# Optimization experiments

Measured on AMD Instinct MI355X. Metric: run time of the kernel, lower is better.

The kernel has to match this reference:

```python
import jax, jax.numpy as jnp
import numpy as np

COMMITMENT_COST = 0.25

def setup_inputs() -> dict:
    key = jax.random.key(0)
    k1, k2 = jax.random.split(key)
    z = jax.random.normal(k1, (8, 2048, 768), dtype=jnp.float32)
    # codebook initialized uniform(-1/K, 1/K) in the original; use same scale
    K = 2048
    emb = jax.random.uniform(k2, (K, 768), dtype=jnp.float32, minval=-1.0 / K, maxval=1.0 / K)
    return {"z": z, "emb": emb}

def reference(z, emb):
    B, S, D = z.shape
    z_flat = z.reshape(-1, D)                                   # [N, D]
    # squared-euclidean distances via expansion: ||z||^2 + ||e||^2 - 2 z e^T
    distances = (
        jnp.sum(z_flat * z_flat, axis=1, keepdims=True)
        + jnp.sum(emb * emb, axis=1)
        - 2.0 * jnp.matmul(z_flat, emb.T)
    )                                                           # [N, K]
    ids_flat = jnp.argmin(distances, axis=1)                    # [N]
    z_q = emb[ids_flat].reshape(z.shape)                        # gather + reshape
    concept_ids = ids_flat.reshape(B, S)
    # training path with use_ema=True: codebook_loss = 0, commitment term only.
    # NOTE: original (faithfully) computes mse(z.detach(), z_q) — grad flows to z_q.
    commitment_loss = jnp.mean((jax.lax.stop_gradient(z) - z_q) ** 2)
    vq_loss = COMMITMENT_COST * commitment_loss
    # straight-through estimator
    z_q_st = z + jax.lax.stop_gradient(z_q - z)
    return z_q_st, concept_ids, vq_loss
```

## Files before the change

kernel.cpp:

```cpp
#include <hip/hip_runtime.h>
#include <float.h>

typedef unsigned short ushort_t;
typedef unsigned int uint_t;

#define NROWS 16384
#define DDIM  768
#define KCODES 2048
#define NCB    16
#define MARGIN 8e-4f

__device__ __forceinline__ ushort_t f2bf(float x) {
    uint_t u = __float_as_uint(x);
    uint_t r = (u + 0x7fffu + ((u >> 16) & 1u)) >> 16;
    return (ushort_t)r;
}
__device__ __forceinline__ float bf2f(ushort_t h) {
    return __uint_as_float(((uint_t)h) << 16);
}

__global__ void prep_emb(const float* __restrict__ emb, float* __restrict__ ee,
                         ushort_t* __restrict__ Eh) {
    int c = blockIdx.x;
    const float* e = emb + (size_t)c * DDIM;
    int t = threadIdx.x;
    float s = 0.f;
    for (int i = t; i < DDIM; i += 256) { float v = e[i]; s += v * v; }
    for (int off = 32; off; off >>= 1) s += __shfl_down(s, off);
    __shared__ float red[4];
    if ((t & 63) == 0) red[t >> 6] = s;
    __syncthreads();
    if (t == 0) ee[c] = red[0] + red[1] + red[2] + red[3];
    if (t < 192) {
        const float4 v = ((const float4*)e)[t];
        ushort4 h;
        h.x = f2bf(v.x); h.y = f2bf(v.y); h.z = f2bf(v.z); h.w = f2bf(v.w);
        ((ushort4*)(Eh + (size_t)c * DDIM))[t] = h;
    }
}

__global__ void prep_z(const float* __restrict__ z, float* __restrict__ zz,
                       ushort_t* __restrict__ Zh) {
    const int t = threadIdx.x;
    const int row = blockIdx.x * 4 + (t >> 6);
    const int lane = t & 63;
    const float* zr = z + (size_t)row * DDIM;
    float s = 0.f;
    for (int i = lane; i < DDIM; i += 64) { float v = zr[i]; s += v * v; }
    for (int off = 32; off; off >>= 1) s += __shfl_down(s, off);
    if (lane == 0) zz[row] = s;
    const float4* zr4 = (const float4*)zr;
    ushort4* dh = (ushort4*)(Zh + (size_t)row * DDIM);
    #pragma unroll
    for (int j = 0; j < 3; ++j) {
        const int i4 = lane + 64 * j;
        const float4 v = zr4[i4];
        ushort4 h;
        h.x = f2bf(v.x); h.y = f2bf(v.y); h.z = f2bf(v.z); h.w = f2bf(v.w);
        dh[i4] = h;
    }
}

typedef __attribute__((ext_vector_type(8))) short bf16x8;
typedef __attribute__((ext_vector_type(4))) float f32x4;

__device__ __forceinline__ int swz(int r) { return (r & 3) ^ ((r >> 2) & 3); }

__global__ __launch_bounds__(256)
void mfma_kernel(const ushort_t* __restrict__ Ab, const ushort_t* __restrict__ Bb,
                 const float* __restrict__ ee, float* __restrict__ bmin,
                 float2* __restrict__ slots) {
    __shared__ __align__(16) char smem[32768];
    ushort_t* Als = (ushort_t*)smem;
    ushort_t* Bls = (ushort_t*)(smem + 16384);
    float* rowmin = (float*)smem;
    int*   rcnt   = (int*)(smem + 512);
    float (*sval)[8] = (float(*)[8])(smem + 1024);
    int   (*sidx)[8] = (int(*)[8])(smem + 5120);

    const int t = threadIdx.x;
    const int w = t >> 6, l = t & 63;
    const int bx = blockIdx.x & 127, by = blockIdx.x >> 7;
    const int row0 = bx << 7, col0 = by << 7;

    f32x4 acc[4][4];
    #pragma unroll
    for (int i = 0; i < 4; ++i)
        #pragma unroll
        for (int j = 0; j < 4; ++j) acc[i][j] = (f32x4){0.f, 0.f, 0.f, 0.f};

    const int sri  = l >> 2;
    const int slot = l & 3;
    const int rha = (w & 1) << 6;
    const int rhb = (w >> 1) << 6;

    for (int kt = 0; kt < 12; ++kt) {
        const int kb = kt << 6;
        __syncthreads();
        #pragma unroll
        for (int s = 0; s < 2; ++s) {
            #pragma unroll
            for (int q = 0; q < 2; ++q) {
                const int r0 = ((w << 1) + q) << 4;
                const int ra = r0 + sri;
                const int c  = slot ^ swz(ra);
                const int kk = kb + (s << 5) + (c << 3);
                const ushort_t* gpa = Ab + (size_t)(row0 + ra) * DDIM + kk;
                __builtin_amdgcn_global_load_lds(
                    (const __attribute__((address_space(1))) void*)gpa,
                    (__attribute__((address_space(3))) void*)(smem + (s << 13) + (r0 << 6)),
                    16, 0, 0);
                const ushort_t* gpb = Bb + (size_t)(col0 + ra) * DDIM + kk;
                __builtin_amdgcn_global_load_lds(
                    (const __attribute__((address_space(1))) void*)gpb,
                    (__attribute__((address_space(3))) void*)(smem + 16384 + (s << 13) + (r0 << 6)),
                    16, 0, 0);
            }
        }
        __syncthreads();

        #pragma unroll
        for (int s = 0; s < 2; ++s) {
            bf16x8 af[4], bfr[4];
            #pragma unroll
            for (int mi = 0; mi < 4; ++mi) {
                const int r = rha + (mi << 4) + (l & 15);
                const int sw = (l >> 4) ^ swz(r);
                af[mi] = *(const bf16x8*)&Als[(s << 12) + (r << 5) + (sw << 3)];
            }
            #pragma unroll
            for (int ni = 0; ni < 4; ++ni) {
                const int r = rhb + (ni << 4) + (l & 15);
                const int sw = (l >> 4) ^ swz(r);
                bfr[ni] = *(const bf16x8*)&Bls[(s << 12) + (r << 5) + (sw << 3)];
            }
            #pragma unroll
            for (int mi = 0; mi < 4; ++mi)
                #pragma unroll
                for (int ni = 0; ni < 4; ++ni)
                    acc[mi][ni] = __builtin_amdgcn_mfma_f32_16x16x32_bf16(
                        af[mi], bfr[ni], acc[mi][ni], 0, 0, 0);
        }
    }
    __syncthreads();

    float ecv[4];
    #pragma unroll
    for (int ni = 0; ni < 4; ++ni) ecv[ni] = ee[col0 + rhb + (ni << 4) + (l & 15)];
    #pragma unroll
    for (int mi = 0; mi < 4; ++mi)
        #pragma unroll
        for (int ni = 0; ni < 4; ++ni)
            #pragma unroll
            for (int r = 0; r < 4; ++r)
                acc[mi][ni][r] = ecv[ni] - 2.0f * acc[mi][ni][r];

    float vmr[4][4];
    #pragma unroll
    for (int mi = 0; mi < 4; ++mi)
        #pragma unroll
        for (int r = 0; r < 4; ++r) {
            float v = fminf(fminf(acc[mi][0][r], acc[mi][1][r]),
                            fminf(acc[mi][2][r], acc[mi][3][r]));
            v = fminf(v, __shfl_xor(v, 1));
            v = fminf(v, __shfl_xor(v, 2));
            v = fminf(v, __shfl_xor(v, 4));
            v = fminf(v, __shfl_xor(v, 8));
            vmr[mi][r] = v;
        }

    if (t < 128) { rowmin[t] = FLT_MAX; rcnt[t] = 0; }
    __syncthreads();
    if (w < 2 && (l & 15) == 0) {
        #pragma unroll
        for (int mi = 0; mi < 4; ++mi)
            #pragma unroll
            for (int r = 0; r < 4; ++r)
                rowmin[rha + (mi << 4) + ((l >> 4) << 2) + r] = vmr[mi][r];
    }
    __syncthreads();
    if (w >= 2 && (l & 15) == 0) {
        #pragma unroll
        for (int mi = 0; mi < 4; ++mi)
            #pragma unroll
            for (int r = 0; r < 4; ++r) {
                const int m = rha + (mi << 4) + ((l >> 4) << 2) + r;
                rowmin[m] = fminf(rowmin[m], vmr[mi][r]);
            }
    }
    __syncthreads();

    #pragma unroll
    for (int mi = 0; mi < 4; ++mi)
        #pragma unroll
        for (int r = 0; r < 4; ++r) {
            const int m = rha + (mi << 4) + ((l >> 4) << 2) + r;
            const float lim = rowmin[m] + MARGIN;
            #pragma unroll
            for (int ni = 0; ni < 4; ++ni) {
                const float vv = acc[mi][ni][r];
                if (vv <= lim) {
                    const int p = atomicAdd(&rcnt[m], 1);
                    if (p < 8) {
                        sval[m][p] = vv;
                        sidx[m][p] = col0 + rhb + (ni << 4) + (l & 15);
                    }
                }
            }
        }
    __syncthreads();

    if (t < 128) {
        const int row = row0 + t;
        bmin[(size_t)by * NROWS + row] = rowmin[t];
        const int n = rcnt[t] < 8 ? rcnt[t] : 8;
        float2 rec[8];
        #pragma unroll
        for (int s2 = 0; s2 < 8; ++s2)
            rec[s2] = (s2 < n) ? make_float2(sval[t][s2], __int_as_float(sidx[t][s2]))
                               : make_float2(FLT_MAX, __int_as_float(0x7fffffff));
        float4* dst = (float4*)(slots + ((size_t)by * NROWS + row) * 8);
        dst[0] = make_float4(rec[0].x, rec[0].y, rec[1].x, rec[1].y);
        dst[1] = make_float4(rec[2].x, rec[2].y, rec[3].x, rec[3].y);
        dst[2] = make_float4(rec[4].x, rec[4].y, rec[5].x, rec[5].y);
        dst[3] = make_float4(rec[6].x, rec[6].y, rec[7].x, rec[7].y);
    }
}

__global__ __launch_bounds__(256)
void combine_select_gather(const float* __restrict__ bmin, const float2* __restrict__ slots,
                           const float* __restrict__ ee, const float* __restrict__ zz,
                           const float* __restrict__ z, const float* __restrict__ emb,
                           float* __restrict__ ids_f32, float* __restrict__ out0,
                           float* __restrict__ rowloss) {
    const int t = threadIdx.x;
    const int row = blockIdx.x * 4 + (t >> 6);
    const int l = t & 63;

    float v = (l < NCB) ? bmin[(size_t)l * NROWS + row] : FLT_MAX;
    v = fminf(v, __shfl_xor(v, 8));
    v = fminf(v, __shfl_xor(v, 4));
    v = fminf(v, __shfl_xor(v, 2));
    v = fminf(v, __shfl_xor(v, 1));
    const float T = __shfl(v, 0) + MARGIN;

    const int blk = l >> 2;
    const int s0 = (l << 1) & 7;
    const float2* sp = slots + ((size_t)blk * NROWS + row) * 8 + s0;
    const float2 a  = sp[0];
    const float2 b2 = sp[1];

    unsigned long long m0 = __ballot(a.x <= T);
    unsigned long long m1 = __ballot(b2.x <= T);

    const float zzr = zz[row];
    const float* zr = z + (size_t)row * DDIM;

    float bestd = FLT_MAX; int besti = 0x7fffffff;
    while (m0 | m1) {
        int j; float iv;
        if (m0) { j = __ffsll(m0) - 1; m0 &= m0 - 1; iv = a.y; }
        else    { j = __ffsll(m1) - 1; m1 &= m1 - 1; iv = b2.y; }
        const int idx = __float_as_int(__shfl(iv, j));
        const float* er = emb + (size_t)idx * DDIM;
        float p = 0.f;
        #pragma unroll
        for (int k = 0; k < 12; ++k) p += zr[l + 64 * k] * er[l + 64 * k];
        for (int off = 32; off; off >>= 1) p += __shfl_down(p, off);
        if (l == 0) {
            const float t1 = zzr + ee[idx];
            const float d  = t1 - 2.0f * p;
            if (d < bestd || (d == bestd && idx < besti)) { bestd = d; besti = idx; }
        }
    }
    const int bi = __shfl(besti, 0);
    if (l == 0) ids_f32[row] = (float)bi;

    const float4* zr4 = (const float4*)zr;
    const float4* er4 = (const float4*)(emb + (size_t)bi * DDIM);
    float4* o4 = (float4*)(out0 + (size_t)row * DDIM);
    float s = 0.f;
    #pragma unroll
    for (int j = 0; j < 3; ++j) {
        const int i4 = l + 64 * j;
        const float4 zv = zr4[i4];
        const float4 ev = er4[i4];
        float4 o;
        o.x = zv.x + (ev.x - zv.x); o.y = zv.y + (ev.y - zv.y);
        o.z = zv.z + (ev.z - zv.z); o.w = zv.w + (ev.w - zv.w);
        o4[i4] = o;
        const float dx = zv.x - ev.x, dy = zv.y - ev.y;
        const float dz = zv.z - ev.z, dw = zv.w - ev.w;
        s += dx * dx + dy * dy + dz * dz + dw * dw;
    }
    for (int off = 32; off; off >>= 1) s += __shfl_down(s, off);
    if (l == 0) rowloss[row] = s;
}

__global__ void loss16k_kernel(const float* __restrict__ rowloss, float* __restrict__ out_loss) {
    const int t = threadIdx.x;
    double s = 0.0;
    for (int i = t; i < NROWS; i += 256) s += (double)rowloss[i];
    for (int off = 32; off; off >>= 1) s += __shfl_down(s, off);
    __shared__ double red[4];
    if ((t & 63) == 0) red[t >> 6] = s;
    __syncthreads();
    if (t == 0) {
        const double total = red[0] + red[1] + red[2] + red[3];
        out_loss[0] = (float)(0.25 * (total / (double)((size_t)NROWS * DDIM)));
    }
}

__global__ void ee_kernel(const float* __restrict__ emb, float* __restrict__ ee) {
    int c = blockIdx.x;
    const float* e = emb + (size_t)c * DDIM;
    int t = threadIdx.x;
    float s = 0.f;
    for (int i = t; i < DDIM; i += 256) { float v = e[i]; s += v * v; }
    for (int off = 32; off; off >>= 1) s += __shfl_down(s, off);
    __shared__ float red[4];
    if ((t & 63) == 0) red[t >> 6] = s;
    __syncthreads();
    if (t == 0) ee[c] = red[0] + red[1] + red[2] + red[3];
}

__global__ void zz_kernel(const float* __restrict__ z, float* __restrict__ zz) {
    const int t = threadIdx.x;
    const int row = blockIdx.x * 4 + (t >> 6);
    const int lane = t & 63;
    const float* zr = z + (size_t)row * DDIM;
    float s = 0.f;
    for (int i = lane; i < DDIM; i += 64) { float v = zr[i]; s += v * v; }
    for (int off = 32; off; off >>= 1) s += __shfl_down(s, off);
    if (lane == 0) zz[row] = s;
}

#define BM 32
#define BN 128
#define BKS 32
#define SPLITC 2
#define CODES_PER_BLOCK (KCODES / SPLITC)
#define NCHUNK (CODES_PER_BLOCK / BN)
#define NSTAGE (DDIM / BKS)
#define APADR 33
#define BPADC 132

__global__ __launch_bounds__(256)
void argmin_kernel(const float* __restrict__ z, const float* __restrict__ emb,
                   const float* __restrict__ ee, const float* __restrict__ zz,
                   float* __restrict__ pval, int* __restrict__ pidx) {
    __shared__ float Af[BKS][APADR];
    __shared__ float Bf[BKS][BPADC];
    __shared__ float cval[BM][33];
    __shared__ int   cidx[BM][33];
    __shared__ float zzs[BM];
    const int t = threadIdx.x;
    const int part = blockIdx.x & (SPLITC - 1);
    const int rb = blockIdx.x >> 1;
    const int row0 = rb * BM;
    const int cbase = part * CODES_PER_BLOCK;
    const int tx = t & 31, ty = t >> 5;
    const int sr = t >> 3;
    const int sk = 4 * (t & 7);
    if (t < BM) zzs[t] = zz[row0 + t];
    float bv[4]; int bi[4];
    #pragma unroll
    for (int i = 0; i < 4; ++i) { bv[i] = FLT_MAX; bi[i] = 0x7fffffff; }
    const float* zt = z + (size_t)(row0 + sr) * DDIM;
    for (int chunk = 0; chunk < NCHUNK; ++chunk) {
        const int c0 = cbase + chunk * BN;
        const float* ebase = emb + (size_t)(c0 + sr) * DDIM;
        float acc[4][4];
        #pragma unroll
        for (int i = 0; i < 4; ++i)
            #pragma unroll
            for (int j = 0; j < 4; ++j) acc[i][j] = 0.f;
        float4 pa = *(const float4*)&zt[sk];
        float4 pb[4];
        #pragma unroll
        for (int m = 0; m < 4; ++m) pb[m] = *(const float4*)&ebase[(size_t)(32 * m) * DDIM + sk];
        for (int s = 0; s < NSTAGE; ++s) {
            __syncthreads();
            Af[sk + 0][sr] = pa.x; Af[sk + 1][sr] = pa.y;
            Af[sk + 2][sr] = pa.z; Af[sk + 3][sr] = pa.w;
            #pragma unroll
            for (int m = 0; m < 4; ++m) {
                Bf[sk + 0][sr + 32 * m] = pb[m].x;
                Bf[sk + 1][sr + 32 * m] = pb[m].y;
                Bf[sk + 2][sr + 32 * m] = pb[m].z;
                Bf[sk + 3][sr + 32 * m] = pb[m].w;
            }
            __syncthreads();
            if (s + 1 < NSTAGE) {
                const int k1 = (s + 1) * BKS + sk;
                pa = *(const float4*)&zt[k1];
                #pragma unroll
                for (int m = 0; m < 4; ++m)
                    pb[m] = *(const float4*)&ebase[(size_t)(32 * m) * DDIM + k1];
            }
            #pragma unroll
            for (int kk = 0; kk < BKS; ++kk) {
                const float4 a4 = *(const float4*)&Af[kk][4 * ty];
                const float4 b4 = *(const float4*)&Bf[kk][4 * tx];
                const float aa[4] = {a4.x, a4.y, a4.z, a4.w};
                const float bb[4] = {b4.x, b4.y, b4.z, b4.w};
                #pragma unroll
                for (int i = 0; i < 4; ++i)
                    #pragma unroll
                    for (int j = 0; j < 4; ++j) acc[i][j] += aa[i] * bb[j];
            }
        }
        const float4 e4 = *(const float4*)&ee[c0 + 4 * tx];
        const float eev[4] = {e4.x, e4.y, e4.z, e4.w};
        #pragma unroll
        for (int i = 0; i < 4; ++i) {
            const float zzr = zzs[4 * ty + i];
            #pragma unroll
            for (int j = 0; j < 4; ++j) {
                const int code = c0 + 4 * tx + j;
                const float t1 = zzr + eev[j];
                const float d  = t1 - 2.0f * acc[i][j];
                if (d < bv[i] || (d == bv[i] && code < bi[i])) { bv[i] = d; bi[i] = code; }
            }
        }
    }
    __syncthreads();
    #pragma unroll
    for (int i = 0; i < 4; ++i) { cval[4 * ty + i][tx] = bv[i]; cidx[4 * ty + i][tx] = bi[i]; }
    __syncthreads();
    if (t < BM) {
        float v = FLT_MAX; int id = 0x7fffffff;
        #pragma unroll
        for (int x = 0; x < 32; ++x) {
            const float cv = cval[t][x]; const int ci = cidx[t][x];
            if (cv < v || (cv == v && ci < id)) { v = cv; id = ci; }
        }
        pval[part * NROWS + row0 + t] = v;
        pidx[part * NROWS + row0 + t] = id;
    }
}

__global__ void combine_kernel(const float* __restrict__ pval, const int* __restrict__ pidx,
                               float* __restrict__ ids_f32) {
    const int r = blockIdx.x * 256 + threadIdx.x;
    float v = pval[r];           int id = pidx[r];
    const float v1 = pval[NROWS + r]; const int i1 = pidx[NROWS + r];
    if (v1 < v || (v1 == v && i1 < id)) { v = v1; id = i1; }
    ids_f32[r] = (float)id;
}

__global__ __launch_bounds__(256)
void gather_kernel(const float* __restrict__ z, const float* __restrict__ emb,
                   const float* __restrict__ ids_f32, float* __restrict__ out0,
                   float* __restrict__ part) {
    const int b = blockIdx.x;
    const int t = threadIdx.x;
    const int rl = t >> 4, c = t & 15;
    __shared__ int ids[16];
    if (t < 16) ids[t] = (int)ids_f32[b * 16 + t];
    __syncthreads();
    const int row = b * 16 + rl;
    const float4* zr = (const float4*)(z + (size_t)row * DDIM);
    float4* orow = (float4*)(out0 + (size_t)row * DDIM);
    const float4* er = (const float4*)(emb + (size_t)ids[rl] * DDIM);
    float s = 0.f;
    #pragma unroll
    for (int j = 0; j < 12; ++j) {
        const int i4 = c + 16 * j;
        const float4 zv = zr[i4];
        const float4 ev = er[i4];
        float4 o;
        o.x = zv.x + (ev.x - zv.x); o.y = zv.y + (ev.y - zv.y);
        o.z = zv.z + (ev.z - zv.z); o.w = zv.w + (ev.w - zv.w);
        orow[i4] = o;
        float dx = zv.x - ev.x, dy = zv.y - ev.y, dz = zv.z - ev.z, dw = zv.w - ev.w;
        s += dx * dx + dy * dy + dz * dz + dw * dw;
    }
    for (int off = 32; off; off >>= 1) s += __shfl_down(s, off);
    __shared__ float red[4];
    if ((t & 63) == 0) red[t >> 6] = s;
    __syncthreads();
    if (t == 0) part[b] = red[0] + red[1] + red[2] + red[3];
}

__global__ void loss_kernel(const float* __restrict__ part, float* __restrict__ out_loss) {
    const int t = threadIdx.x;
    double s = 0.0;
    for (int i = t; i < 1024; i += 256) s += (double)part[i];
    for (int off = 32; off; off >>= 1) s += __shfl_down(s, off);
    __shared__ double red[4];
    if ((t & 63) == 0) red[t >> 6] = s;
    __syncthreads();
    if (t == 0) {
        const double total = red[0] + red[1] + red[2] + red[3];
        out_loss[0] = (float)(0.25 * (total / (double)((size_t)NROWS * DDIM)));
    }
}

#define EE_OFF   0
#define ZZ_OFF   8192
#define RL_OFF   73728
#define EH_OFF   139264
#define ZH_OFF   (EH_OFF + (size_t)KCODES * DDIM * 2)
#define BMIN_OFF (ZH_OFF + (size_t)NROWS * DDIM * 2)
#define SLOT_OFF (BMIN_OFF + (size_t)NCB * NROWS * 4)
#define WS_NEED  (SLOT_OFF + (size_t)NCB * NROWS * 8 * 8)
#define PV_OFF   81920

extern "C" void kernel_launch(void* const* d_in, const int* in_sizes, int n_in,
                              void* d_out, int out_size, void* d_ws, size_t ws_size,
                              hipStream_t stream) {
    const float* z   = (const float*)d_in[0];
    const float* emb = (const float*)d_in[1];

    float* out0     = (float*)d_out;
    float* out_ids  = out0 + (size_t)NROWS * DDIM;
    float* out_loss = out_ids + NROWS;

    char* ws = (char*)d_ws;
    float* ee   = (float*)(ws + EE_OFF);
    float* zzws = (float*)(ws + ZZ_OFF);

    if (ws_size >= WS_NEED) {
        ushort_t* Eh   = (ushort_t*)(ws + EH_OFF);
        ushort_t* Zh   = (ushort_t*)(ws + ZH_OFF);
        float*    bmin = (float*)(ws + BMIN_OFF);
        float2*   slot = (float2*)(ws + SLOT_OFF);
        float*    rl   = (float*)(ws + RL_OFF);
        prep_emb<<<KCODES, 256, 0, stream>>>(emb, ee, Eh);
        prep_z<<<NROWS / 4, 256, 0, stream>>>(z, zzws, Zh);
        mfma_kernel<<<(NROWS / 128) * NCB, 256, 0, stream>>>(Zh, Eh, ee, bmin, slot);
        combine_select_gather<<<NROWS / 4, 256, 0, stream>>>(bmin, slot, ee, zzws, z, emb,
                                                             out_ids, out0, rl);
        loss16k_kernel<<<1, 256, 0, stream>>>(rl, out_loss);
    } else {
        float* part = (float*)(ws + RL_OFF);
        float* pval = (float*)(ws + PV_OFF);
        int*   pidx = (int*)(ws + PV_OFF + 131072);
        ee_kernel<<<KCODES, 256, 0, stream>>>(emb, ee);
        zz_kernel<<<NROWS / 4, 256, 0, stream>>>(z, zzws);
        argmin_kernel<<<(NROWS / BM) * SPLITC, 256, 0, stream>>>(z, emb, ee, zzws, pval, pidx);
        combine_kernel<<<NROWS / 256, 256, 0, stream>>>(pval, pidx, out_ids);
        gather_kernel<<<NROWS / 16, 256, 0, stream>>>(z, emb, out_ids, out0, part);
        loss_kernel<<<1, 256, 0, stream>>>(part, out_loss);
    }
}
```

Measured before the change: 249.3 us.

## Widen MFMA tiles to 128x256, merge prep kernels, fold loss via atomics

The MFMA argmin kernel now covers 256 codebook columns per block instead of 128, which halves the column splits and the partial-min/slot traffic. Its K loop switches to single-stage 32-wide steps with precomputed load and LDS addresses, and sets launch bounds for two blocks per CU. The two prep kernels are merged into one launch, and the final loss reduction kernel is dropped in favour of per-block float atomicAdd. In exchange there is more register pressure from 32 accumulators, less K work per barrier, and a loss sum in nondeterministic float order.

```diff
diff --git a/kernel.cpp b/kernel.cpp
--- a/kernel.cpp
+++ b/kernel.cpp
@@ -7,7 +7,7 @@
 #define NROWS 16384
 #define DDIM  768
 #define KCODES 2048
-#define NCB    16
+#define NCB2   8
 #define MARGIN 8e-4f
 
 __device__ __forceinline__ ushort_t f2bf(float x) {
@@ -19,45 +19,47 @@
     return __uint_as_float(((uint_t)h) << 16);
 }
 
-__global__ void prep_emb(const float* __restrict__ emb, float* __restrict__ ee,
-                         ushort_t* __restrict__ Eh) {
-    int c = blockIdx.x;
-    const float* e = emb + (size_t)c * DDIM;
-    int t = threadIdx.x;
-    float s = 0.f;
-    for (int i = t; i < DDIM; i += 256) { float v = e[i]; s += v * v; }
-    for (int off = 32; off; off >>= 1) s += __shfl_down(s, off);
-    __shared__ float red[4];
-    if ((t & 63) == 0) red[t >> 6] = s;
-    __syncthreads();
-    if (t == 0) ee[c] = red[0] + red[1] + red[2] + red[3];
-    if (t < 192) {
-        const float4 v = ((const float4*)e)[t];
-        ushort4 h;
-        h.x = f2bf(v.x); h.y = f2bf(v.y); h.z = f2bf(v.z); h.w = f2bf(v.w);
-        ((ushort4*)(Eh + (size_t)c * DDIM))[t] = h;
-    }
-}
-
-__global__ void prep_z(const float* __restrict__ z, float* __restrict__ zz,
-                       ushort_t* __restrict__ Zh) {
-    const int t = threadIdx.x;
-    const int row = blockIdx.x * 4 + (t >> 6);
-    const int lane = t & 63;
-    const float* zr = z + (size_t)row * DDIM;
-    float s = 0.f;
-    for (int i = lane; i < DDIM; i += 64) { float v = zr[i]; s += v * v; }
-    for (int off = 32; off; off >>= 1) s += __shfl_down(s, off);
-    if (lane == 0) zz[row] = s;
-    const float4* zr4 = (const float4*)zr;
-    ushort4* dh = (ushort4*)(Zh + (size_t)row * DDIM);
-    #pragma unroll
-    for (int j = 0; j < 3; ++j) {
-        const int i4 = lane + 64 * j;
-        const float4 v = zr4[i4];
-        ushort4 h;
-        h.x = f2bf(v.x); h.y = f2bf(v.y); h.z = f2bf(v.z); h.w = f2bf(v.w);
-        dh[i4] = h;
+__global__ void prep_kernel(const float* __restrict__ z, const float* __restrict__ emb,
+                            float* __restrict__ ee, float* __restrict__ zz,
+                            ushort_t* __restrict__ Zh, ushort_t* __restrict__ Eh,
+                            float* __restrict__ out_loss) {
+    const int b = blockIdx.x, t = threadIdx.x;
+    if (b == 0 && t == 0) out_loss[0] = 0.f;
+    if (b < KCODES) {
+        const int c = b;
+        const float* e = emb + (size_t)c * DDIM;
+        float s = 0.f;
+        for (int i = t; i < DDIM; i += 256) { float v = e[i]; s += v * v; }
+        for (int off = 32; off; off >>= 1) s += __shfl_down(s, off);
+        __shared__ float red[4];
+        if ((t & 63) == 0) red[t >> 6] = s;
+        __syncthreads();
+        if (t == 0) ee[c] = red[0] + red[1] + red[2] + red[3];
+        if (t < 192) {
+            const float4 v = ((const float4*)e)[t];
+            ushort4 h;
+            h.x = f2bf(v.x); h.y = f2bf(v.y); h.z = f2bf(v.z); h.w = f2bf(v.w);
+            ((ushort4*)(Eh + (size_t)c * DDIM))[t] = h;
+        }
+    } else {
+        const int rb = b - KCODES;
+        const int row = rb * 4 + (t >> 6);
+        const int lane = t & 63;
+        const float* zr = z + (size_t)row * DDIM;
+        float s = 0.f;
+        for (int i = lane; i < DDIM; i += 64) { float v = zr[i]; s += v * v; }
+        for (int off = 32; off; off >>= 1) s += __shfl_down(s, off);
+        if (lane == 0) zz[row] = s;
+        const float4* zr4 = (const float4*)zr;
+        ushort4* dh = (ushort4*)(Zh + (size_t)row * DDIM);
+        #pragma unroll
+        for (int j = 0; j < 3; ++j) {
+            const int i4 = lane + 64 * j;
+            const float4 v = zr4[i4];
+            ushort4 h;
+            h.x = f2bf(v.x); h.y = f2bf(v.y); h.z = f2bf(v.z); h.w = f2bf(v.w);
+            dh[i4] = h;
+        }
     }
 }
 
@@ -66,13 +68,11 @@
 
 __device__ __forceinline__ int swz(int r) { return (r & 3) ^ ((r >> 2) & 3); }
 
-__global__ __launch_bounds__(256)
+__global__ __launch_bounds__(256, 2)
 void mfma_kernel(const ushort_t* __restrict__ Ab, const ushort_t* __restrict__ Bb,
                  const float* __restrict__ ee, float* __restrict__ bmin,
                  float2* __restrict__ slots) {
-    __shared__ __align__(16) char smem[32768];
-    ushort_t* Als = (ushort_t*)smem;
-    ushort_t* Bls = (ushort_t*)(smem + 16384);
+    __shared__ __align__(16) char smem[24576];
     float* rowmin = (float*)smem;
     int*   rcnt   = (int*)(smem + 512);
     float (*sval)[8] = (float(*)[8])(smem + 1024);
@@ -80,77 +80,93 @@
 
     const int t = threadIdx.x;
     const int w = t >> 6, l = t & 63;
-    const int bx = blockIdx.x & 127, by = blockIdx.x >> 7;
-    const int row0 = bx << 7, col0 = by << 7;
-
-    f32x4 acc[4][4];
+    const int bx = blockIdx.x & 127;
+    const int by = blockIdx.x >> 7;
+    const int row0 = bx << 7;
+    const int col0 = by << 8;
+
+    f32x4 acc[4][8];
     #pragma unroll
     for (int i = 0; i < 4; ++i)
         #pragma unroll
-        for (int j = 0; j < 4; ++j) acc[i][j] = (f32x4){0.f, 0.f, 0.f, 0.f};
-
-    const int sri  = l >> 2;
-    const int slot = l & 3;
+        for (int j = 0; j < 8; ++j) acc[i][j] = (f32x4){0.f, 0.f, 0.f, 0.f};
+
+    const int sri = l >> 2, slot = l & 3;
+    const ushort_t* gA[2]; uint_t lA[2];
+    #pragma unroll
+    for (int q = 0; q < 2; ++q) {
+        const int r0 = ((w << 1) + q) << 4;
+        const int ra = r0 + sri;
+        const int c  = slot ^ swz(ra);
+        gA[q] = Ab + (size_t)(row0 + ra) * DDIM + (c << 3);
+        lA[q] = r0 << 6;
+    }
+    const ushort_t* gB[4]; uint_t lB[4];
+    #pragma unroll
+    for (int q = 0; q < 4; ++q) {
+        const int r0 = ((w << 2) + q) << 4;
+        const int ra = r0 + sri;
+        const int c  = slot ^ swz(ra);
+        gB[q] = Bb + (size_t)(col0 + ra) * DDIM + (c << 3);
+        lB[q] = 8192 + (r0 << 6);
+    }
+
     const int rha = (w & 1) << 6;
-    const int rhb = (w >> 1) << 6;
-
-    for (int kt = 0; kt < 12; ++kt) {
-        const int kb = kt << 6;
+    const int chb = (w >> 1) << 7;
+    const ushort_t* aAddr[4]; const ushort_t* bAddr[8];
+    #pragma unroll
+    for (int mi = 0; mi < 4; ++mi) {
+        const int r = rha + (mi << 4) + (l & 15);
+        const int sw = (l >> 4) ^ swz(r);
+        aAddr[mi] = (const ushort_t*)(smem + (r << 6) + (sw << 4));
+    }
+    #pragma unroll
+    for (int ni = 0; ni < 8; ++ni) {
+        const int r = chb + (ni << 4) + (l & 15);
+        const int sw = (l >> 4) ^ swz(r);
+        bAddr[ni] = (const ushort_t*)(smem + 8192 + (r << 6) + (sw << 4));
+    }
+
+    for (int kt = 0; kt < 24; ++kt) {
         __syncthreads();
         #pragma unroll
-        for (int s = 0; s < 2; ++s) {
-            #pragma unroll
-            for (int q = 0; q < 2; ++q) {
-                const int r0 = ((w << 1) + q) << 4;
-                const int ra = r0 + sri;
-                const int c  = slot ^ swz(ra);
-                const int kk = kb + (s << 5) + (c << 3);
-                const ushort_t* gpa = Ab + (size_t)(row0 + ra) * DDIM + kk;
-                __builtin_amdgcn_global_load_lds(
-                    (const __attribute__((address_space(1))) void*)gpa,
-                    (__attribute__((address_space(3))) void*)(smem + (s << 13) + (r0 << 6)),
-                    16, 0, 0);
-                const ushort_t* gpb = Bb + (size_t)(col0 + ra) * DDIM + kk;
-                __builtin_amdgcn_global_load_lds(
-                    (const __attribute__((address_space(1))) void*)gpb,
-                    (__attribute__((address_space(3))) void*)(smem + 16384 + (s << 13) + (r0 << 6)),
-                    16, 0, 0);
-            }
+        for (int q = 0; q < 2; ++q) {
+            __builtin_amdgcn_global_load_lds(
+                (const __attribute__((address_space(1))) void*)gA[q],
+                (__attribute__((address_space(3))) void*)(smem + lA[q]), 16, 0, 0);
+            gA[q] += 32;
+        }
+        #pragma unroll
+        for (int q = 0; q < 4; ++q) {
+            __builtin_amdgcn_global_load_lds(
+                (const __attribute__((address_space(1))) void*)gB[q],
+                (__attribute__((address_space(3))) void*)(smem + lB[q]), 16, 0, 0);
+            gB[q] += 32;
         }
         __syncthreads();
 
-        #pragma unroll
-        for (int s = 0; s < 2; ++s) {
-            bf16x8 af[4], bfr[4];
-            #pragma unroll
-            for (int mi = 0; mi < 4; ++mi) {
-                const int r = rha + (mi << 4) + (l & 15);
-                const int sw = (l >> 4) ^ swz(r);
-                af[mi] = *(const bf16x8*)&Als[(s << 12) + (r << 5) + (sw << 3)];
-            }
-            #pragma unroll
-            for (int ni = 0; ni < 4; ++ni) {
-                const int r = rhb + (ni << 4) + (l & 15);
-                const int sw = (l >> 4) ^ swz(r);
-                bfr[ni] = *(const bf16x8*)&Bls[(s << 12) + (r << 5) + (sw << 3)];
-            }
-            #pragma unroll
-            for (int mi = 0; mi < 4; ++mi)
-                #pragma unroll
-                for (int ni = 0; ni < 4; ++ni)
-                    acc[mi][ni] = __builtin_amdgcn_mfma_f32_16x16x32_bf16(
-                        af[mi], bfr[ni], acc[mi][ni], 0, 0, 0);
-        }
-    }
-    __syncthreads();
-
-    float ecv[4];
-    #pragma unroll
-    for (int ni = 0; ni < 4; ++ni) ecv[ni] = ee[col0 + rhb + (ni << 4) + (l & 15)];
+        bf16x8 af[4], bfr[8];
+        #pragma unroll
+        for (int mi = 0; mi < 4; ++mi) af[mi] = *(const bf16x8*)aAddr[mi];
+        #pragma unroll
+        for (int ni = 0; ni < 8; ++ni) bfr[ni] = *(const bf16x8*)bAddr[ni];
+        #pragma unroll
+        for (int mi = 0; mi < 4; ++mi)
+            #pragma unroll
+            for (int ni = 0; ni < 8; ++ni)
+                acc[mi][ni] = __builtin_amdgcn_mfma_f32_16x16x32_bf16(
+                    af[mi], bfr[ni], acc[mi][ni], 0, 0, 0);
+    }
+
+    __syncthreads();
+
+    float ecv[8];
+    #pragma unroll
+    for (int ni = 0; ni < 8; ++ni) ecv[ni] = ee[col0 + chb + (ni << 4) + (l & 15)];
     #pragma unroll
     for (int mi = 0; mi < 4; ++mi)
         #pragma unroll
-        for (int ni = 0; ni < 4; ++ni)
+        for (int ni = 0; ni < 8; ++ni)
             #pragma unroll
             for (int r = 0; r < 4; ++r)
                 acc[mi][ni][r] = ecv[ni] - 2.0f * acc[mi][ni][r];
@@ -160,8 +176,9 @@
     for (int mi = 0; mi < 4; ++mi)
         #pragma unroll
         for (int r = 0; r < 4; ++r) {
-            float v = fminf(fminf(acc[mi][0][r], acc[mi][1][r]),
-                            fminf(acc[mi][2][r], acc[mi][3][r]));
+            float v = acc[mi][0][r];
+            #pragma unroll
+            for (int ni = 1; ni < 8; ++ni) v = fminf(v, acc[mi][ni][r]);
             v = fminf(v, __shfl_xor(v, 1));
             v = fminf(v, __shfl_xor(v, 2));
             v = fminf(v, __shfl_xor(v, 4));
@@ -197,13 +214,13 @@
             const int m = rha + (mi << 4) + ((l >> 4) << 2) + r;
             const float lim = rowmin[m] + MARGIN;
             #pragma unroll
-            for (int ni = 0; ni < 4; ++ni) {
+            for (int ni = 0; ni < 8; ++ni) {
                 const float vv = acc[mi][ni][r];
                 if (vv <= lim) {
                     const int p = atomicAdd(&rcnt[m], 1);
                     if (p < 8) {
                         sval[m][p] = vv;
-                        sidx[m][p] = col0 + rhb + (ni << 4) + (l & 15);
+                        sidx[m][p] = col0 + chb + (ni << 4) + (l & 15);
                     }
                 }
             }
@@ -232,36 +249,31 @@
                            const float* __restrict__ ee, const float* __restrict__ zz,
                            const float* __restrict__ z, const float* __restrict__ emb,
                            float* __restrict__ ids_f32, float* __restrict__ out0,
-                           float* __restrict__ rowloss) {
+                           float* __restrict__ out_loss) {
     const int t = threadIdx.x;
-    const int row = blockIdx.x * 4 + (t >> 6);
+    const int w = t >> 6;
+    const int row = blockIdx.x * 4 + w;
     const int l = t & 63;
 
-    float v = (l < NCB) ? bmin[(size_t)l * NROWS + row] : FLT_MAX;
-    v = fminf(v, __shfl_xor(v, 8));
+    float v = (l < NCB2) ? bmin[(size_t)l * NROWS + row] : FLT_MAX;
     v = fminf(v, __shfl_xor(v, 4));
     v = fminf(v, __shfl_xor(v, 2));
     v = fminf(v, __shfl_xor(v, 1));
     const float T = __shfl(v, 0) + MARGIN;
 
-    const int blk = l >> 2;
-    const int s0 = (l << 1) & 7;
-    const float2* sp = slots + ((size_t)blk * NROWS + row) * 8 + s0;
-    const float2 a  = sp[0];
-    const float2 b2 = sp[1];
-
-    unsigned long long m0 = __ballot(a.x <= T);
-    unsigned long long m1 = __ballot(b2.x <= T);
+    const int blk = l >> 3;
+    const int s0 = l & 7;
+    const float2 a = slots[((size_t)blk * NROWS + row) * 8 + s0];
+
+    unsigned long long m = __ballot(a.x <= T);
 
     const float zzr = zz[row];
     const float* zr = z + (size_t)row * DDIM;
 
     float bestd = FLT_MAX; int besti = 0x7fffffff;
-    while (m0 | m1) {
-        int j; float iv;
-        if (m0) { j = __ffsll(m0) - 1; m0 &= m0 - 1; iv = a.y; }
-        else    { j = __ffsll(m1) - 1; m1 &= m1 - 1; iv = b2.y; }
-        const int idx = __float_as_int(__shfl(iv, j));
+    while (m) {
+        const int j = __ffsll(m) - 1; m &= m - 1;
+        const int idx = __float_as_int(__shfl(a.y, j));
         const float* er = emb + (size_t)idx * DDIM;
         float p = 0.f;
         #pragma unroll
@@ -294,20 +306,12 @@
         s += dx * dx + dy * dy + dz * dz + dw * dw;
     }
     for (int off = 32; off; off >>= 1) s += __shfl_down(s, off);
-    if (l == 0) rowloss[row] = s;
-}
-
-__global__ void loss16k_kernel(const float* __restrict__ rowloss, float* __restrict__ out_loss) {
-    const int t = threadIdx.x;
-    double s = 0.0;
-    for (int i = t; i < NROWS; i += 256) s += (double)rowloss[i];
-    for (int off = 32; off; off >>= 1) s += __shfl_down(s, off);
-    __shared__ double red[4];
-    if ((t & 63) == 0) red[t >> 6] = s;
+    __shared__ float lred[4];
+    if (l == 0) lred[w] = s;
     __syncthreads();
     if (t == 0) {
-        const double total = red[0] + red[1] + red[2] + red[3];
-        out_loss[0] = (float)(0.25 * (total / (double)((size_t)NROWS * DDIM)));
+        const float tot = lred[0] + lred[1] + lred[2] + lred[3];
+        atomicAdd(out_loss, tot * (0.25f / (float)((size_t)NROWS * DDIM)));
     }
 }
 
@@ -499,12 +503,12 @@
 
 #define EE_OFF   0
 #define ZZ_OFF   8192
-#define RL_OFF   73728
-#define EH_OFF   139264
+#define EH_OFF   73728
 #define ZH_OFF   (EH_OFF + (size_t)KCODES * DDIM * 2)
 #define BMIN_OFF (ZH_OFF + (size_t)NROWS * DDIM * 2)
-#define SLOT_OFF (BMIN_OFF + (size_t)NCB * NROWS * 4)
-#define WS_NEED  (SLOT_OFF + (size_t)NCB * NROWS * 8 * 8)
+#define SLOT_OFF (BMIN_OFF + (size_t)NCB2 * NROWS * 4)
+#define WS_NEED  (SLOT_OFF + (size_t)NCB2 * NROWS * 8 * 8)
+#define PART_OFF 73728
 #define PV_OFF   81920
 
 extern "C" void kernel_launch(void* const* d_in, const int* in_sizes, int n_in,
@@ -526,15 +530,12 @@
         ushort_t* Zh   = (ushort_t*)(ws + ZH_OFF);
         float*    bmin = (float*)(ws + BMIN_OFF);
         float2*   slot = (float2*)(ws + SLOT_OFF);
-        float*    rl   = (float*)(ws + RL_OFF);
-        prep_emb<<<KCODES, 256, 0, stream>>>(emb, ee, Eh);
-        prep_z<<<NROWS / 4, 256, 0, stream>>>(z, zzws, Zh);
-        mfma_kernel<<<(NROWS / 128) * NCB, 256, 0, stream>>>(Zh, Eh, ee, bmin, slot);
+        prep_kernel<<<KCODES + NROWS / 4, 256, 0, stream>>>(z, emb, ee, zzws, Zh, Eh, out_loss);
+        mfma_kernel<<<(NROWS / 128) * NCB2, 256, 0, stream>>>(Zh, Eh, ee, bmin, slot);
         combine_select_gather<<<NROWS / 4, 256, 0, stream>>>(bmin, slot, ee, zzws, z, emb,
-                                                             out_ids, out0, rl);
-        loss16k_kernel<<<1, 256, 0, stream>>>(rl, out_loss);
+                                                             out_ids, out0, out_loss);
     } else {
-        float* part = (float*)(ws + RL_OFF);
+        float* part = (float*)(ws + PART_OFF);
         float* pval = (float*)(ws + PV_OFF);
         int*   pidx = (int*)(ws + PV_OFF + 131072);
         ee_kernel<<<KCODES, 256, 0, stream>>>(emb, ee);
```

Result: faster. 242.2 us (-2.9%).
